# Kernel optimization log

Hardware: AMD Instinct MI355X
Metric: run time of the kernel (lower is better)

## Reference

```python
import jax, jax.numpy as jnp
import numpy as np

NB = 2        # trm_num_blocks
H = 4         # trm_num_heads
D = 128       # trm_hidden_dim
L = 512
B = 1
PAD = 0
NEG = jnp.float32(-2**32 + 1)


def _ln(x, g, b, eps=1e-8):
    m = x.mean(-1, keepdims=True)
    v = x.var(-1, keepdims=True)
    return (x - m) / jnp.sqrt(v + eps) * g + b


def setup_inputs() -> dict:
    key = jax.random.key(0)
    ks = jax.random.split(key, 16)
    s = 0.02
    inp = {
        "log_seqs": jax.random.randint(ks[0], (B, L), 0, 1000),
        "seqs": jax.random.normal(ks[1], (B, L, D), jnp.float32),
        "time_matrix_K": jax.random.normal(ks[2], (B, L, L, D), jnp.float32),
        # per-block stacked params [NB, ...]
        "Wq": jax.random.normal(ks[3], (NB, D, D), jnp.float32) * s,
        "bq": jnp.zeros((NB, D), jnp.float32),
        "Wk": jax.random.normal(ks[4], (NB, D, D), jnp.float32) * s,
        "bk": jnp.zeros((NB, D), jnp.float32),
        "Wv": jax.random.normal(ks[5], (NB, D, D), jnp.float32) * s,
        "bv": jnp.zeros((NB, D), jnp.float32),
        "Wt": jax.random.normal(ks[6], (NB, D, D), jnp.float32) * s,
        "bt": jnp.zeros((NB, D), jnp.float32),
        "Wtp": jax.random.normal(ks[7], (NB, D, 1), jnp.float32) * s,
        "btp": jnp.zeros((NB, 1), jnp.float32),
        "ln1_g": jnp.ones((NB, D), jnp.float32),
        "ln1_b": jnp.zeros((NB, D), jnp.float32),
        "ln2_g": jnp.ones((NB, D), jnp.float32),
        "ln2_b": jnp.zeros((NB, D), jnp.float32),
        "W1": jax.random.normal(ks[8], (NB, D, D), jnp.float32) * s,
        "b1": jnp.zeros((NB, D), jnp.float32),
        "W2": jax.random.normal(ks[9], (NB, D, D), jnp.float32) * s,
        "b2": jnp.zeros((NB, D), jnp.float32),
        "lnf_g": jnp.ones((D,), jnp.float32),
        "lnf_b": jnp.zeros((D,), jnp.float32),
    }
    return inp


def reference(log_seqs, seqs, time_matrix_K, Wq, bq, Wk, bk, Wv, bv, Wt, bt,
              Wtp, btp, ln1_g, ln1_b, ln2_g, ln2_b, W1, b1, W2, b2, lnf_g, lnf_b):
    hd = D // H
    pad = (log_seqs == PAD)                     # [B, L] True at padding
    keep = (~pad)[..., None].astype(seqs.dtype)  # [B, L, 1]
    seqs = seqs * keep
    causal = ~jnp.tril(jnp.ones((L, L), bool))  # True above diagonal (masked)
    # combined mask [1, B, L, L]: pad query rows OR non-causal entries
    mask = pad[None, :, :, None] | causal[None, None, :, :]

    attn_ws = []
    for i in range(NB):
        Q = _ln(seqs, ln1_g[i], ln1_b[i])
        q = Q @ Wq[i] + bq[i]
        k = seqs @ Wk[i] + bk[i]
        v = seqs @ Wv[i] + bv[i]
        # head-major layout [H, B, L, hd] (matches torch split+cat along dim 0)
        qh = q.reshape(B, L, H, hd).transpose(2, 0, 1, 3)
        kh = k.reshape(B, L, H, hd).transpose(2, 0, 1, 3)
        vh = v.reshape(B, L, H, hd).transpose(2, 0, 1, 3)
        scores = jnp.einsum('hbqd,hbkd->hbqk', qh, kh)  # [H, B, L, L]
        # time bias: sigmoid(proj(relu(W_t t))) in (0,1); log is negative
        tw = jax.nn.sigmoid(
            (jax.nn.relu(time_matrix_K @ Wt[i] + bt[i]) @ Wtp[i] + btp[i]).squeeze(-1)
        )                                             # [B, L, L]
        scores = (scores + jnp.log(tw)) / jnp.float32(hd) ** 0.5
        scores = jnp.where(mask, NEG, scores)
        w = jax.nn.softmax(scores, axis=-1)           # dropout is identity (eval)
        attn_ws.append(w.reshape(H * B, L, L))
        out = jnp.einsum('hbqk,hbkd->hbqd', w, vh).transpose(1, 2, 0, 3).reshape(B, L, D)
        seqs = Q + out
        x = _ln(seqs, ln2_g[i], ln2_b[i])
        y = jax.nn.relu(x @ W1[i] + b1[i]) @ W2[i] + b2[i]
        seqs = (x + y) * keep                         # FFN residual adds post-LN x
    log_feats = _ln(seqs, lnf_g, lnf_b)
    return (log_feats, tuple(attn_ws))
```

## Files before the change

kernel.cpp:

```cpp
#include <hip/hip_runtime.h>

#define L 512
#define D 128
#define H 4
#define HD 32
#define XLD 132

typedef __bf16 bf16x8 __attribute__((ext_vector_type(8)));
typedef float  f32x4  __attribute__((ext_vector_type(4)));

__device__ __forceinline__ unsigned short bfbits(float v){
  __bf16 h = (__bf16)v; unsigned short u; __builtin_memcpy(&u, &h, 2); return u;
}
__device__ __forceinline__ bf16x8 cvt8(float4 a0, float4 a1){
  bf16x8 r;
  r[0] = (__bf16)a0.x; r[1] = (__bf16)a0.y; r[2] = (__bf16)a0.z; r[3] = (__bf16)a0.w;
  r[4] = (__bf16)a1.x; r[5] = (__bf16)a1.y; r[6] = (__bf16)a1.z; r[7] = (__bf16)a1.w;
  return r;
}

__device__ __forceinline__ void write_qA(unsigned short* qA, int row, int c, float v){
  int qt = row >> 4, m = row & 15;
  int h = c >> 5, cc = c & 31;
  qA[(((qt * 4 + h) * 64) + (cc >> 3) * 16 + m) * 8 + (cc & 7)] = bfbits(v);
}
__device__ __forceinline__ void write_kB(unsigned short* kB, int row, int c, float v){
  int h = c >> 5, cc = c & 31;
  int nt = row >> 4;
  kB[((h * 32 + nt) * 64 + (cc >> 3) * 16 + (row & 15)) * 8 + (cc & 7)] = bfbits(v);
}
__device__ __forceinline__ void write_vB(unsigned short* vB, int row, int c, float v){
  int h = c >> 5, cc = c & 31;
  int kk = row >> 5, qv = (row >> 3) & 3, jv = row & 7;
  int nt = cc >> 4;
  vB[(((h * 16 + kk) * 2 + nt) * 64 + qv * 16 + (cc & 15)) * 8 + jv] = bfbits(v);
}

__device__ __forceinline__ void row_stats16(const float (*buf)[XLD], int tid,
                                            float* mean_s, float* rstd_s){
  int row_l = tid >> 4, seg = tid & 15;
  const float* p = &buf[row_l][seg * 8];
  float4 f0 = *(const float4*)p, f1 = *(const float4*)(p + 4);
  float sum = f0.x + f0.y + f0.z + f0.w + f1.x + f1.y + f1.z + f1.w;
  float sq  = f0.x*f0.x + f0.y*f0.y + f0.z*f0.z + f0.w*f0.w
            + f1.x*f1.x + f1.y*f1.y + f1.z*f1.z + f1.w*f1.w;
#pragma unroll
  for (int o = 1; o < 16; o <<= 1){ sum += __shfl_xor(sum, o); sq += __shfl_xor(sq, o); }
  if (seg == 0){
    float mn = sum * (1.f / 128.f);
    mean_s[row_l] = mn;
    rstd_s[row_l] = rsqrtf(fmaxf(sq * (1.f / 128.f) - mn * mn, 0.f) + 1e-8f);
  }
}

__device__ __forceinline__ void build_afr(const float (*buf)[XLD], int lane, bf16x8* afr){
  int m = lane & 15, quad = lane >> 4;
#pragma unroll
  for (int k0 = 0; k0 < 4; ++k0){
    const float* p = &buf[m][k0 * 32 + quad * 8];
    afr[k0] = cvt8(*(const float4*)p, *(const float4*)(p + 4));
  }
}
__device__ __forceinline__ void build_afr_ln(const float (*buf)[XLD], int lane,
    const float* mean_s, const float* rstd_s,
    const float* __restrict__ g, const float* __restrict__ b, bf16x8* afr){
  int m = lane & 15, quad = lane >> 4;
  float mn = mean_s[m], rs = rstd_s[m];
#pragma unroll
  for (int k0 = 0; k0 < 4; ++k0){
    int c0 = k0 * 32 + quad * 8;
    const float* p = &buf[m][c0];
    float4 a0 = *(const float4*)p, a1 = *(const float4*)(p + 4);
    float q[8];
    q[0]=(a0.x-mn)*rs*g[c0+0]+b[c0+0]; q[1]=(a0.y-mn)*rs*g[c0+1]+b[c0+1];
    q[2]=(a0.z-mn)*rs*g[c0+2]+b[c0+2]; q[3]=(a0.w-mn)*rs*g[c0+3]+b[c0+3];
    q[4]=(a1.x-mn)*rs*g[c0+4]+b[c0+4]; q[5]=(a1.y-mn)*rs*g[c0+5]+b[c0+5];
    q[6]=(a1.z-mn)*rs*g[c0+6]+b[c0+6]; q[7]=(a1.w-mn)*rs*g[c0+7]+b[c0+7];
    bf16x8 r;
    r[0]=(__bf16)q[0]; r[1]=(__bf16)q[1]; r[2]=(__bf16)q[2]; r[3]=(__bf16)q[3];
    r[4]=(__bf16)q[4]; r[5]=(__bf16)q[5]; r[6]=(__bf16)q[6]; r[7]=(__bf16)q[7];
    afr[k0] = r;
  }
}

__global__ void k_prep(const float* __restrict__ Wt,
                       const float* __restrict__ Wq, const float* __restrict__ Wk,
                       const float* __restrict__ Wv, const float* __restrict__ W1,
                       const float* __restrict__ W2,
                       unsigned short* __restrict__ bfg, unsigned short* __restrict__ wf){
  int idx = blockIdx.x * 256 + threadIdx.x;
  if (idx < 32768){
    int jj   = idx & 7;
    int lane = (idx >> 3) & 63;
    int k0   = (idx >> 9) & 3;
    int nt   = idx >> 11;
    int d    = k0 * 32 + (lane >> 4) * 8 + jj;
    int col  = (nt & 7) * 16 + (lane & 15);
    int blk  = nt >> 3;
    bfg[idx] = bfbits(Wt[blk * D * D + d * D + col]);
  } else {
    int i2 = idx - 32768;
    int jj = i2 & 7, lane = (i2 >> 3) & 63, k0 = (i2 >> 9) & 3, nt = (i2 >> 11) & 7;
    int mat = i2 >> 14;
    int blk = mat / 5, m5 = mat % 5;
    const float* W = (m5 == 0 ? Wq : m5 == 1 ? Wk : m5 == 2 ? Wv : m5 == 3 ? W1 : W2)
                     + blk * D * D;
    int d = k0 * 32 + (lane >> 4) * 8 + jj;
    int col = nt * 16 + (lane & 15);
    wf[i2] = bfbits(W[d * D + col]);
  }
}

__global__ __launch_bounds__(256, 2) void k_timebias(
    const float* __restrict__ T, const unsigned short* __restrict__ bfg,
    const float* __restrict__ bt, const float* __restrict__ wtp,
    const float* __restrict__ btp, float* __restrict__ logtw){
  __shared__ __align__(16) unsigned short bsh[16384];
  __shared__ float bts[128], wtps[128];
  int tid = threadIdx.x;
  int lane = tid & 63, w = tid >> 6;
  int quad = lane >> 4, m = lane & 15;
  const bf16x8* bls = (const bf16x8*)bsh;
  int wbase = blockIdx.x * 256 + w * 64;

  bf16x8 afr[4][4];
#pragma unroll
  for (int mt = 0; mt < 4; ++mt){
    const float* tp = T + (size_t)(wbase + mt * 16 + m) * D + quad * 8;
#pragma unroll
    for (int k0 = 0; k0 < 4; ++k0){
      float4 f0 = *(const float4*)(tp + k0 * 32);
      float4 f1 = *(const float4*)(tp + k0 * 32 + 4);
      afr[mt][k0] = cvt8(f0, f1);
    }
  }

#pragma unroll
  for (int blk = 0; blk < 2; ++blk){
    if (blk) __syncthreads();
    {
      const uint4* g = (const uint4*)(bfg + blk * 16384);
      uint4* s = (uint4*)bsh;
#pragma unroll
      for (int i = 0; i < 8; ++i) s[tid + i * 256] = g[tid + i * 256];
      if (tid < 128){ bts[tid] = bt[blk * 128 + tid]; wtps[tid] = wtp[blk * 128 + tid]; }
    }
    __syncthreads();

    f32x4 rs[4] = {{0,0,0,0},{0,0,0,0},{0,0,0,0},{0,0,0,0}};
#pragma unroll
    for (int ntl = 0; ntl < 8; ++ntl){
      f32x4 acc[4] = {{0,0,0,0},{0,0,0,0},{0,0,0,0},{0,0,0,0}};
#pragma unroll
      for (int k0 = 0; k0 < 4; ++k0){
        bf16x8 b = bls[(ntl * 4 + k0) * 64 + lane];
#pragma unroll
        for (int mt = 0; mt < 4; ++mt)
          acc[mt] = __builtin_amdgcn_mfma_f32_16x16x32_bf16(afr[mt][k0], b, acc[mt], 0, 0, 0);
      }
      float btv = bts[ntl * 16 + m];
      float wtv = wtps[ntl * 16 + m];
#pragma unroll
      for (int mt = 0; mt < 4; ++mt)
#pragma unroll
        for (int r = 0; r < 4; ++r)
          rs[mt][r] += fmaxf(acc[mt][r] + btv, 0.f) * wtv;
    }
#pragma unroll
    for (int mt = 0; mt < 4; ++mt)
#pragma unroll
      for (int r = 0; r < 4; ++r){
        float v = rs[mt][r];
        v += __shfl_xor(v, 1); v += __shfl_xor(v, 2);
        v += __shfl_xor(v, 4); v += __shfl_xor(v, 8);
        rs[mt][r] = v;
      }
    if (m == 0){
      float bp = btp[blk];
      float* out = logtw + blk * (L * L);
#pragma unroll
      for (int mt = 0; mt < 4; ++mt){
        float4 o;
        float s0 = rs[mt][0] + bp; o.x = -__logf(1.f + __expf(-s0));
        float s1 = rs[mt][1] + bp; o.y = -__logf(1.f + __expf(-s1));
        float s2 = rs[mt][2] + bp; o.z = -__logf(1.f + __expf(-s2));
        float s3 = rs[mt][3] + bp; o.w = -__logf(1.f + __expf(-s3));
        *(float4*)(out + wbase + mt * 16 + quad * 4) = o;
      }
    }
  }
}

__global__ __launch_bounds__(256) void k_qkv_m(
    const float* __restrict__ src, const int* __restrict__ ls, int domask,
    const float* __restrict__ g1, const float* __restrict__ b1,
    const unsigned short* __restrict__ wf, int matq,
    const float* __restrict__ bq, const float* __restrict__ bk,
    const float* __restrict__ bv,
    float* __restrict__ Q, unsigned short* __restrict__ qA,
    unsigned short* __restrict__ kB, unsigned short* __restrict__ vB){
  __shared__ float xs[16][XLD];
  __shared__ float mean_s[16], rstd_s[16];
  __shared__ float g1s[128], b1s[128];
  int tid = threadIdx.x, rowbase = blockIdx.x * 16;
  int mat = blockIdx.y;
  int row_l = tid >> 4, seg = tid & 15;

  const float* sp = src + (rowbase + row_l) * D + seg * 8;
  float4 f0 = *(const float4*)sp, f1 = *(const float4*)(sp + 4);
  if (domask && ls[rowbase + row_l] == 0){
    f0 = make_float4(0,0,0,0); f1 = make_float4(0,0,0,0);
  }
  *(float4*)&xs[row_l][seg * 8] = f0;
  *(float4*)&xs[row_l][seg * 8 + 4] = f1;
  if (mat == 0 && tid < 128){ g1s[tid] = g1[tid]; b1s[tid] = b1[tid]; }
  __syncthreads();
  if (mat == 0){
    row_stats16(xs, tid, mean_s, rstd_s);
    __syncthreads();
    float mn = mean_s[row_l], rs = rstd_s[row_l];
    float* qp = Q + (rowbase + row_l) * D + seg * 8;
    float4 o0, o1;
    int c0 = seg * 8;
    o0.x=(f0.x-mn)*rs*g1s[c0+0]+b1s[c0+0]; o0.y=(f0.y-mn)*rs*g1s[c0+1]+b1s[c0+1];
    o0.z=(f0.z-mn)*rs*g1s[c0+2]+b1s[c0+2]; o0.w=(f0.w-mn)*rs*g1s[c0+3]+b1s[c0+3];
    o1.x=(f1.x-mn)*rs*g1s[c0+4]+b1s[c0+4]; o1.y=(f1.y-mn)*rs*g1s[c0+5]+b1s[c0+5];
    o1.z=(f1.z-mn)*rs*g1s[c0+6]+b1s[c0+6]; o1.w=(f1.w-mn)*rs*g1s[c0+7]+b1s[c0+7];
    *(float4*)qp = o0; *(float4*)(qp + 4) = o1;
  }

  int lane = tid & 63, w = tid >> 6;
  int quad = lane >> 4, mcol = lane & 15;
  bf16x8 afr[4];
  if (mat == 0) build_afr_ln(xs, lane, mean_s, rstd_s, g1s, b1s, afr);
  else          build_afr(xs, lane, afr);

  const float* bias_v = (mat == 0 ? bq : mat == 1 ? bk : bv);
#pragma unroll
  for (int jl = 0; jl < 2; ++jl){
    int nt = w * 2 + jl;
    const bf16x8* wfb = (const bf16x8*)wf + ((size_t)(matq + mat) * 8 + nt) * 4 * 64;
    f32x4 acc = {0, 0, 0, 0};
#pragma unroll
    for (int k0 = 0; k0 < 4; ++k0)
      acc = __builtin_amdgcn_mfma_f32_16x16x32_bf16(afr[k0], wfb[k0 * 64 + lane], acc, 0, 0, 0);
    int c = nt * 16 + mcol;
    float bias = bias_v[c];
#pragma unroll
    for (int r = 0; r < 4; ++r){
      int row = rowbase + quad * 4 + r;
      float v = acc[r] + bias;
      if (mat == 0) write_qA(qA, row, c, v);
      else if (mat == 1) write_kB(kB, row, c, v);
      else write_vB(vB, row, c, v);
    }
  }
}

__global__ __launch_bounds__(256) void k_attn(
    const unsigned short* __restrict__ qA, const unsigned short* __restrict__ kB,
    const unsigned short* __restrict__ vB, const float* __restrict__ logtw,
    const int* __restrict__ ls, const float* __restrict__ Q,
    float* __restrict__ wout, float* __restrict__ xr){
  __shared__ __align__(16) unsigned short pa[16 * 64 * 8];
  __shared__ float pvp[4][2][64][4];
  __shared__ float smax[4][16], ssum[4][16];
  int qt = blockIdx.x >> 2, h = blockIdx.x & 3;
  int tid = threadIdx.x, lane = tid & 63, w = tid >> 6;
  int quad = lane >> 4, mcol = lane & 15;
  const float RS = 0.17677669529663687f;

  bf16x8 qf = ((const bf16x8*)qA)[(qt * 4 + h) * 64 + lane];

  f32x4 acc[8];
#pragma unroll
  for (int nt8 = 0; nt8 < 8; ++nt8){
    bf16x8 bf = ((const bf16x8*)kB)[(h * 32 + w * 8 + nt8) * 64 + lane];
    f32x4 z = {0, 0, 0, 0};
    acc[nt8] = __builtin_amdgcn_mfma_f32_16x16x32_bf16(qf, bf, z, 0, 0, 0);
  }

  float e[8][4];
  float mx4[4] = {-3e38f, -3e38f, -3e38f, -3e38f};
#pragma unroll
  for (int nt8 = 0; nt8 < 8; ++nt8){
    int col = w * 128 + nt8 * 16 + mcol;
#pragma unroll
    for (int r = 0; r < 4; ++r){
      int row = qt * 16 + quad * 4 + r;
      float sv = (acc[nt8][r] + logtw[row * L + col]) * RS;
      sv = (col <= row) ? sv : -3e38f;
      e[nt8][r] = sv;
      mx4[r] = fmaxf(mx4[r], sv);
    }
  }
#pragma unroll
  for (int r = 0; r < 4; ++r){
    float v = mx4[r];
    v = fmaxf(v, __shfl_xor(v, 1)); v = fmaxf(v, __shfl_xor(v, 2));
    v = fmaxf(v, __shfl_xor(v, 4)); v = fmaxf(v, __shfl_xor(v, 8));
    mx4[r] = v;
  }
  if (mcol == 0){
#pragma unroll
    for (int r = 0; r < 4; ++r) smax[w][quad * 4 + r] = mx4[r];
  }
  __syncthreads();
  float mxr[4], sum4[4] = {0, 0, 0, 0};
#pragma unroll
  for (int r = 0; r < 4; ++r){
    int rr = quad * 4 + r;
    mxr[r] = fmaxf(fmaxf(smax[0][rr], smax[1][rr]), fmaxf(smax[2][rr], smax[3][rr]));
  }
#pragma unroll
  for (int nt8 = 0; nt8 < 8; ++nt8)
#pragma unroll
    for (int r = 0; r < 4; ++r){
      float sv = e[nt8][r];
      float ev = (sv > -1e38f) ? __expf(sv - mxr[r]) : 0.f;
      e[nt8][r] = ev;
      sum4[r] += ev;
    }
#pragma unroll
  for (int r = 0; r < 4; ++r){
    float v = sum4[r];
    v += __shfl_xor(v, 1); v += __shfl_xor(v, 2);
    v += __shfl_xor(v, 4); v += __shfl_xor(v, 8);
    sum4[r] = v;
  }
  if (mcol == 0){
#pragma unroll
    for (int r = 0; r < 4; ++r) ssum[w][quad * 4 + r] = sum4[r];
  }
  __syncthreads();
  float inv[4]; int padr[4];
#pragma unroll
  for (int r = 0; r < 4; ++r){
    int rr = quad * 4 + r;
    inv[r] = 1.f / (ssum[0][rr] + ssum[1][rr] + ssum[2][rr] + ssum[3][rr]);
    padr[r] = (ls[qt * 16 + rr] == 0);
  }
#pragma unroll
  for (int nt8 = 0; nt8 < 8; ++nt8){
    int col = w * 128 + nt8 * 16 + mcol;
    int kk = col >> 5, qk = (col >> 3) & 3, jj = col & 7;
#pragma unroll
    for (int r = 0; r < 4; ++r){
      int rl = quad * 4 + r;
      float wv = padr[r] ? (1.f / 512.f) : e[nt8][r] * inv[r];
      wout[h * (L * L) + (qt * 16 + rl) * L + col] = wv;
      pa[(kk * 64 + qk * 16 + rl) * 8 + jj] = bfbits(wv);
    }
  }

  f32x4 pacc[2] = {{0,0,0,0},{0,0,0,0}};
#pragma unroll
  for (int kk4 = 0; kk4 < 4; ++kk4){
    int kk = w * 4 + kk4;
    bf16x8 af = ((const bf16x8*)pa)[kk * 64 + lane];
#pragma unroll
    for (int nt = 0; nt < 2; ++nt){
      bf16x8 bf = ((const bf16x8*)vB)[((h * 16 + kk) * 2 + nt) * 64 + lane];
      pacc[nt] = __builtin_amdgcn_mfma_f32_16x16x32_bf16(af, bf, pacc[nt], 0, 0, 0);
    }
  }
#pragma unroll
  for (int nt = 0; nt < 2; ++nt)
#pragma unroll
    for (int r = 0; r < 4; ++r) pvp[w][nt][lane][r] = pacc[nt][r];
  __syncthreads();
  if (w < 2){
    int nt = w;
#pragma unroll
    for (int r = 0; r < 4; ++r){
      float o = pvp[0][nt][lane][r] + pvp[1][nt][lane][r]
              + pvp[2][nt][lane][r] + pvp[3][nt][lane][r];
      int row = qt * 16 + quad * 4 + r;
      int cg = h * HD + nt * 16 + mcol;
      xr[row * D + cg] = Q[row * D + cg] + o;
    }
  }
}

__global__ __launch_bounds__(256) void k_ffn_m(
    const float* __restrict__ xr, const int* __restrict__ ls,
    const float* __restrict__ g2, const float* __restrict__ b2,
    const unsigned short* __restrict__ wf, int mat1,
    const float* __restrict__ b1f, const float* __restrict__ b2f,
    int fuse_qkv, const float* __restrict__ g1, const float* __restrict__ b1,
    int matq, const float* __restrict__ bq, const float* __restrict__ bk,
    const float* __restrict__ bv,
    float* __restrict__ Q, unsigned short* __restrict__ qA,
    unsigned short* __restrict__ kB, unsigned short* __restrict__ vB,
    int fuse_lnf, const float* __restrict__ lg, const float* __restrict__ lb,
    float* __restrict__ lf){
  __shared__ float xs[16][XLD];
  __shared__ float x2s[16][XLD];
  __shared__ float y1s[16][XLD];
  __shared__ float xos[16][XLD];
  __shared__ float mean_s[16], rstd_s[16];
  __shared__ float gs[128], bs[128];
  int tid = threadIdx.x, rowbase = blockIdx.x * 16;
  int row_l = tid >> 4, seg = tid & 15;
  int lane = tid & 63, w = tid >> 6;
  int quad = lane >> 4, mcol = lane & 15;

  {
    const float* sp = xr + (rowbase + row_l) * D + seg * 8;
    *(float4*)&xs[row_l][seg * 8] = *(const float4*)sp;
    *(float4*)&xs[row_l][seg * 8 + 4] = *(const float4*)(sp + 4);
    if (tid < 128){ gs[tid] = g2[tid]; bs[tid] = b2[tid]; }
  }
  __syncthreads();
  row_stats16(xs, tid, mean_s, rstd_s);
  __syncthreads();
  {
    float mn = mean_s[row_l], rs = rstd_s[row_l];
#pragma unroll
    for (int i = 0; i < 8; ++i){
      int c = seg * 8 + i;
      x2s[row_l][c] = (xs[row_l][c] - mn) * rs * gs[c] + bs[c];
    }
  }
  __syncthreads();

  bf16x8 afr[4];
  build_afr(x2s, lane, afr);
#pragma unroll
  for (int jl = 0; jl < 2; ++jl){
    int nt = w * 2 + jl;
    const bf16x8* wfb = (const bf16x8*)wf + ((size_t)mat1 * 8 + nt) * 4 * 64;
    f32x4 acc = {0, 0, 0, 0};
#pragma unroll
    for (int k0 = 0; k0 < 4; ++k0)
      acc = __builtin_amdgcn_mfma_f32_16x16x32_bf16(afr[k0], wfb[k0 * 64 + lane], acc, 0, 0, 0);
    int c = nt * 16 + mcol;
    float bias = b1f[c];
#pragma unroll
    for (int r = 0; r < 4; ++r)
      y1s[quad * 4 + r][c] = fmaxf(acc[r] + bias, 0.f);
  }
  __syncthreads();

  build_afr(y1s, lane, afr);
#pragma unroll
  for (int jl = 0; jl < 2; ++jl){
    int nt = w * 2 + jl;
    const bf16x8* wfb = (const bf16x8*)wf + ((size_t)(mat1 + 1) * 8 + nt) * 4 * 64;
    f32x4 acc = {0, 0, 0, 0};
#pragma unroll
    for (int k0 = 0; k0 < 4; ++k0)
      acc = __builtin_amdgcn_mfma_f32_16x16x32_bf16(afr[k0], wfb[k0 * 64 + lane], acc, 0, 0, 0);
    int c = nt * 16 + mcol;
    float bias = b2f[c];
#pragma unroll
    for (int r = 0; r < 4; ++r){
      int rl = quad * 4 + r;
      float kp = (ls[rowbase + rl] != 0) ? 1.f : 0.f;
      xos[rl][c] = (x2s[rl][c] + acc[r] + bias) * kp;
    }
  }
  __syncthreads();

  if (fuse_qkv){
    if (tid < 128){ gs[tid] = g1[tid]; bs[tid] = b1[tid]; }
    row_stats16(xos, tid, mean_s, rstd_s);
    __syncthreads();
    {
      float mn = mean_s[row_l], rs = rstd_s[row_l];
      float* qp = Q + (rowbase + row_l) * D + seg * 8;
      float4 o0, o1;
      int c0 = seg * 8;
      o0.x=(xos[row_l][c0+0]-mn)*rs*gs[c0+0]+bs[c0+0];
      o0.y=(xos[row_l][c0+1]-mn)*rs*gs[c0+1]+bs[c0+1];
      o0.z=(xos[row_l][c0+2]-mn)*rs*gs[c0+2]+bs[c0+2];
      o0.w=(xos[row_l][c0+3]-mn)*rs*gs[c0+3]+bs[c0+3];
      o1.x=(xos[row_l][c0+4]-mn)*rs*gs[c0+4]+bs[c0+4];
      o1.y=(xos[row_l][c0+5]-mn)*rs*gs[c0+5]+bs[c0+5];
      o1.z=(xos[row_l][c0+6]-mn)*rs*gs[c0+6]+bs[c0+6];
      o1.w=(xos[row_l][c0+7]-mn)*rs*gs[c0+7]+bs[c0+7];
      *(float4*)qp = o0; *(float4*)(qp + 4) = o1;
    }
    bf16x8 afrQ[4], afrX[4];
    build_afr_ln(xos, lane, mean_s, rstd_s, gs, bs, afrQ);
    build_afr(xos, lane, afrX);
#pragma unroll
    for (int jl = 0; jl < 6; ++jl){
      int j = w * 6 + jl;
      int mat = j >> 3, nt = j & 7;
      const bf16x8* wfb = (const bf16x8*)wf + ((size_t)(matq + mat) * 8 + nt) * 4 * 64;
      f32x4 acc = {0, 0, 0, 0};
#pragma unroll
      for (int k0 = 0; k0 < 4; ++k0)
        acc = __builtin_amdgcn_mfma_f32_16x16x32_bf16(mat == 0 ? afrQ[k0] : afrX[k0],
                                                      wfb[k0 * 64 + lane], acc, 0, 0, 0);
      int c = nt * 16 + mcol;
      float bias = (mat == 0 ? bq : mat == 1 ? bk : bv)[c];
#pragma unroll
      for (int r = 0; r < 4; ++r){
        int row = rowbase + quad * 4 + r;
        float v = acc[r] + bias;
        if (mat == 0) write_qA(qA, row, c, v);
        else if (mat == 1) write_kB(kB, row, c, v);
        else write_vB(vB, row, c, v);
      }
    }
  }

  if (fuse_lnf){
    if (tid < 128){ gs[tid] = lg[tid]; bs[tid] = lb[tid]; }
    row_stats16(xos, tid, mean_s, rstd_s);
    __syncthreads();
    float mn = mean_s[row_l], rs = rstd_s[row_l];
    float* op = lf + (rowbase + row_l) * D + seg * 8;
    float4 o0, o1;
    int c0 = seg * 8;
    o0.x=(xos[row_l][c0+0]-mn)*rs*gs[c0+0]+bs[c0+0];
    o0.y=(xos[row_l][c0+1]-mn)*rs*gs[c0+1]+bs[c0+1];
    o0.z=(xos[row_l][c0+2]-mn)*rs*gs[c0+2]+bs[c0+2];
    o0.w=(xos[row_l][c0+3]-mn)*rs*gs[c0+3]+bs[c0+3];
    o1.x=(xos[row_l][c0+4]-mn)*rs*gs[c0+4]+bs[c0+4];
    o1.y=(xos[row_l][c0+5]-mn)*rs*gs[c0+5]+bs[c0+5];
    o1.z=(xos[row_l][c0+6]-mn)*rs*gs[c0+6]+bs[c0+6];
    o1.w=(xos[row_l][c0+7]-mn)*rs*gs[c0+7]+bs[c0+7];
    *(float4*)op = o0; *(float4*)(op + 4) = o1;
  }
}

extern "C" void kernel_launch(void* const* d_in, const int* in_sizes, int n_in,
                              void* d_out, int out_size, void* d_ws, size_t ws_size,
                              hipStream_t stream){
  const int*   ls   = (const int*)d_in[0];
  const float* seqs = (const float*)d_in[1];
  const float* T    = (const float*)d_in[2];
  const float* Wq   = (const float*)d_in[3];
  const float* bq   = (const float*)d_in[4];
  const float* Wk   = (const float*)d_in[5];
  const float* bk   = (const float*)d_in[6];
  const float* Wv   = (const float*)d_in[7];
  const float* bv   = (const float*)d_in[8];
  const float* Wt   = (const float*)d_in[9];
  const float* bt   = (const float*)d_in[10];
  const float* Wtp  = (const float*)d_in[11];
  const float* btp  = (const float*)d_in[12];
  const float* g1   = (const float*)d_in[13];
  const float* b1   = (const float*)d_in[14];
  const float* g2   = (const float*)d_in[15];
  const float* b2   = (const float*)d_in[16];
  const float* W1   = (const float*)d_in[17];
  const float* b1f  = (const float*)d_in[18];
  const float* W2   = (const float*)d_in[19];
  const float* b2f  = (const float*)d_in[20];
  const float* lg   = (const float*)d_in[21];
  const float* lb   = (const float*)d_in[22];

  float* ws    = (float*)d_ws;
  float* Q     = ws;
  float* xr    = Q + 65536;
  float* logtw = xr + 65536;
  unsigned short* bfg = (unsigned short*)(logtw + 2 * 262144);
  unsigned short* wf  = bfg + 32768;
  unsigned short* qA  = wf + 163840;
  unsigned short* kB  = qA + 65536;
  unsigned short* vB  = kB + 65536;

  float* outF = (float*)d_out;
  float* lf = outF;
  float* w0 = outF + 65536;
  float* w1 = w0 + 1048576;

  k_prep    <<<768, 256, 0, stream>>>(Wt, Wq, Wk, Wv, W1, W2, bfg, wf);
  k_timebias<<<1024, 256, 0, stream>>>(T, bfg, bt, Wtp, btp, logtw);

  k_qkv_m<<<dim3(32, 3), 256, 0, stream>>>(seqs, ls, 1, g1, b1, wf, 0, bq, bk, bv,
                                           Q, qA, kB, vB);
  k_attn<<<128, 256, 0, stream>>>(qA, kB, vB, logtw, ls, Q, w0, xr);
  k_ffn_m<<<32, 256, 0, stream>>>(xr, ls, g2, b2, wf, 3, b1f, b2f,
                                  1, g1 + D, b1 + D, 5, bq + D, bk + D, bv + D,
                                  Q, qA, kB, vB,
                                  0, lg, lb, lf);
  k_attn<<<128, 256, 0, stream>>>(qA, kB, vB, logtw + L * L, ls, Q, w1, xr);
  k_ffn_m<<<32, 256, 0, stream>>>(xr, ls, g2 + D, b2 + D, wf, 8, b1f + D, b2f + D,
                                  0, g1, b1, 0, bq, bk, bv,
                                  Q, qA, kB, vB,
                                  1, lg, lb, lf);
}
```

Before: 276.6 us.

## Skip masked causal tiles in time-bias and attention; merge time-bias with QKV kernel

The time-bias kernel now computes only the lower-triangular 64-wide key strips. 576 blocks cover the causal region instead of 1024 covering the full L×L grid, so most of the large time_matrix read and the MFMA work above the diagonal are skipped. The first QKV projection is folded into the same launch as extra blocks, removing one kernel launch. In attention, waves whose key range lies entirely above the diagonal skip the QK MFMAs, the logtw loads and the PV MFMAs. The risk is that logtw above the diagonal is left unwritten, which is safe only because those entries are always masked.

```diff
diff --git a/kernel.cpp b/kernel.cpp
--- a/kernel.cpp
+++ b/kernel.cpp
@@ -5,6 +5,7 @@
 #define H 4
 #define HD 32
 #define XLD 132
+#define NTB 576
 
 typedef __bf16 bf16x8 __attribute__((ext_vector_type(8)));
 typedef float  f32x4  __attribute__((ext_vector_type(4)));
@@ -111,104 +112,115 @@
   }
 }
 
-__global__ __launch_bounds__(256, 2) void k_timebias(
+__global__ __launch_bounds__(256, 2) void k_tb_qkv(
     const float* __restrict__ T, const unsigned short* __restrict__ bfg,
     const float* __restrict__ bt, const float* __restrict__ wtp,
-    const float* __restrict__ btp, float* __restrict__ logtw){
-  __shared__ __align__(16) unsigned short bsh[16384];
-  __shared__ float bts[128], wtps[128];
-  int tid = threadIdx.x;
-  int lane = tid & 63, w = tid >> 6;
-  int quad = lane >> 4, m = lane & 15;
-  const bf16x8* bls = (const bf16x8*)bsh;
-  int wbase = blockIdx.x * 256 + w * 64;
-
-  bf16x8 afr[4][4];
-#pragma unroll
-  for (int mt = 0; mt < 4; ++mt){
-    const float* tp = T + (size_t)(wbase + mt * 16 + m) * D + quad * 8;
-#pragma unroll
-    for (int k0 = 0; k0 < 4; ++k0){
-      float4 f0 = *(const float4*)(tp + k0 * 32);
-      float4 f1 = *(const float4*)(tp + k0 * 32 + 4);
-      afr[mt][k0] = cvt8(f0, f1);
-    }
-  }
-
-#pragma unroll
-  for (int blk = 0; blk < 2; ++blk){
-    if (blk) __syncthreads();
-    {
-      const uint4* g = (const uint4*)(bfg + blk * 16384);
-      uint4* s = (uint4*)bsh;
-#pragma unroll
-      for (int i = 0; i < 8; ++i) s[tid + i * 256] = g[tid + i * 256];
-      if (tid < 128){ bts[tid] = bt[blk * 128 + tid]; wtps[tid] = wtp[blk * 128 + tid]; }
-    }
-    __syncthreads();
-
-    f32x4 rs[4] = {{0,0,0,0},{0,0,0,0},{0,0,0,0},{0,0,0,0}};
-#pragma unroll
-    for (int ntl = 0; ntl < 8; ++ntl){
-      f32x4 acc[4] = {{0,0,0,0},{0,0,0,0},{0,0,0,0},{0,0,0,0}};
-#pragma unroll
-      for (int k0 = 0; k0 < 4; ++k0){
-        bf16x8 b = bls[(ntl * 4 + k0) * 64 + lane];
-#pragma unroll
-        for (int mt = 0; mt < 4; ++mt)
-          acc[mt] = __builtin_amdgcn_mfma_f32_16x16x32_bf16(afr[mt][k0], b, acc[mt], 0, 0, 0);
-      }
-      float btv = bts[ntl * 16 + m];
-      float wtv = wtps[ntl * 16 + m];
-#pragma unroll
-      for (int mt = 0; mt < 4; ++mt)
-#pragma unroll
-        for (int r = 0; r < 4; ++r)
-          rs[mt][r] += fmaxf(acc[mt][r] + btv, 0.f) * wtv;
-    }
-#pragma unroll
-    for (int mt = 0; mt < 4; ++mt)
-#pragma unroll
-      for (int r = 0; r < 4; ++r){
-        float v = rs[mt][r];
-        v += __shfl_xor(v, 1); v += __shfl_xor(v, 2);
-        v += __shfl_xor(v, 4); v += __shfl_xor(v, 8);
-        rs[mt][r] = v;
-      }
-    if (m == 0){
-      float bp = btp[blk];
-      float* out = logtw + blk * (L * L);
-#pragma unroll
-      for (int mt = 0; mt < 4; ++mt){
-        float4 o;
-        float s0 = rs[mt][0] + bp; o.x = -__logf(1.f + __expf(-s0));
-        float s1 = rs[mt][1] + bp; o.y = -__logf(1.f + __expf(-s1));
-        float s2 = rs[mt][2] + bp; o.z = -__logf(1.f + __expf(-s2));
-        float s3 = rs[mt][3] + bp; o.w = -__logf(1.f + __expf(-s3));
-        *(float4*)(out + wbase + mt * 16 + quad * 4) = o;
-      }
-    }
-  }
-}
-
-__global__ __launch_bounds__(256) void k_qkv_m(
-    const float* __restrict__ src, const int* __restrict__ ls, int domask,
+    const float* __restrict__ btp, float* __restrict__ logtw,
+    const float* __restrict__ src, const int* __restrict__ ls,
     const float* __restrict__ g1, const float* __restrict__ b1,
-    const unsigned short* __restrict__ wf, int matq,
+    const unsigned short* __restrict__ wf,
     const float* __restrict__ bq, const float* __restrict__ bk,
     const float* __restrict__ bv,
     float* __restrict__ Q, unsigned short* __restrict__ qA,
     unsigned short* __restrict__ kB, unsigned short* __restrict__ vB){
+  __shared__ __align__(16) unsigned short bsh[16384];
+  __shared__ float bts[128], wtps[128];
   __shared__ float xs[16][XLD];
   __shared__ float mean_s[16], rstd_s[16];
   __shared__ float g1s[128], b1s[128];
-  int tid = threadIdx.x, rowbase = blockIdx.x * 16;
-  int mat = blockIdx.y;
+  int tid = threadIdx.x;
+  int lane = tid & 63, w = tid >> 6;
+  int quad = lane >> 4;
+
+  if (blockIdx.x < NTB){
+    int m = lane & 15;
+    const bf16x8* bls = (const bf16x8*)bsh;
+    int strip = blockIdx.x * 4 + w;
+    int b = 0;
+#pragma unroll
+    for (int i = 1; i < 8; ++i) if (strip >= 32 * i * (i + 1)) b = i;
+    int r0 = strip - 32 * b * (b + 1);
+    int q  = b * 64 + r0 / (b + 1);
+    int kb = (r0 % (b + 1)) * 64;
+    int wbase = q * L + kb;
+
+    bf16x8 afr[4][4];
+#pragma unroll
+    for (int mt = 0; mt < 4; ++mt){
+      const float* tp = T + (size_t)(wbase + mt * 16 + m) * D + quad * 8;
+#pragma unroll
+      for (int k0 = 0; k0 < 4; ++k0){
+        float4 f0 = *(const float4*)(tp + k0 * 32);
+        float4 f1 = *(const float4*)(tp + k0 * 32 + 4);
+        afr[mt][k0] = cvt8(f0, f1);
+      }
+    }
+
+#pragma unroll
+    for (int blk = 0; blk < 2; ++blk){
+      if (blk) __syncthreads();
+      {
+        const uint4* g = (const uint4*)(bfg + blk * 16384);
+        uint4* s = (uint4*)bsh;
+#pragma unroll
+        for (int i = 0; i < 8; ++i) s[tid + i * 256] = g[tid + i * 256];
+        if (tid < 128){ bts[tid] = bt[blk * 128 + tid]; wtps[tid] = wtp[blk * 128 + tid]; }
+      }
+      __syncthreads();
+
+      f32x4 rs[4] = {{0,0,0,0},{0,0,0,0},{0,0,0,0},{0,0,0,0}};
+#pragma unroll
+      for (int ntl = 0; ntl < 8; ++ntl){
+        f32x4 acc[4] = {{0,0,0,0},{0,0,0,0},{0,0,0,0},{0,0,0,0}};
+#pragma unroll
+        for (int k0 = 0; k0 < 4; ++k0){
+          bf16x8 bfr = bls[(ntl * 4 + k0) * 64 + lane];
+#pragma unroll
+          for (int mt = 0; mt < 4; ++mt)
+            acc[mt] = __builtin_amdgcn_mfma_f32_16x16x32_bf16(afr[mt][k0], bfr, acc[mt], 0, 0, 0);
+        }
+        float btv = bts[ntl * 16 + m];
+        float wtv = wtps[ntl * 16 + m];
+#pragma unroll
+        for (int mt = 0; mt < 4; ++mt)
+#pragma unroll
+          for (int r = 0; r < 4; ++r)
+            rs[mt][r] += fmaxf(acc[mt][r] + btv, 0.f) * wtv;
+      }
+#pragma unroll
+      for (int mt = 0; mt < 4; ++mt)
+#pragma unroll
+        for (int r = 0; r < 4; ++r){
+          float v = rs[mt][r];
+          v += __shfl_xor(v, 1); v += __shfl_xor(v, 2);
+          v += __shfl_xor(v, 4); v += __shfl_xor(v, 8);
+          rs[mt][r] = v;
+        }
+      if (m == 0){
+        float bp = btp[blk];
+        float* out = logtw + blk * (L * L);
+#pragma unroll
+        for (int mt = 0; mt < 4; ++mt){
+          float4 o;
+          float s0 = rs[mt][0] + bp; o.x = -__logf(1.f + __expf(-s0));
+          float s1 = rs[mt][1] + bp; o.y = -__logf(1.f + __expf(-s1));
+          float s2 = rs[mt][2] + bp; o.z = -__logf(1.f + __expf(-s2));
+          float s3 = rs[mt][3] + bp; o.w = -__logf(1.f + __expf(-s3));
+          *(float4*)(out + wbase + mt * 16 + quad * 4) = o;
+        }
+      }
+    }
+    return;
+  }
+
+  int bi = blockIdx.x - NTB;
+  int rowbase = (bi & 31) * 16;
+  int mat = bi >> 5;
   int row_l = tid >> 4, seg = tid & 15;
 
   const float* sp = src + (rowbase + row_l) * D + seg * 8;
   float4 f0 = *(const float4*)sp, f1 = *(const float4*)(sp + 4);
-  if (domask && ls[rowbase + row_l] == 0){
+  if (ls[rowbase + row_l] == 0){
     f0 = make_float4(0,0,0,0); f1 = make_float4(0,0,0,0);
   }
   *(float4*)&xs[row_l][seg * 8] = f0;
@@ -229,8 +241,7 @@
     *(float4*)qp = o0; *(float4*)(qp + 4) = o1;
   }
 
-  int lane = tid & 63, w = tid >> 6;
-  int quad = lane >> 4, mcol = lane & 15;
+  int mcol = lane & 15;
   bf16x8 afr[4];
   if (mat == 0) build_afr_ln(xs, lane, mean_s, rstd_s, g1s, b1s, afr);
   else          build_afr(xs, lane, afr);
@@ -239,7 +250,7 @@
 #pragma unroll
   for (int jl = 0; jl < 2; ++jl){
     int nt = w * 2 + jl;
-    const bf16x8* wfb = (const bf16x8*)wf + ((size_t)(matq + mat) * 8 + nt) * 4 * 64;
+    const bf16x8* wfb = (const bf16x8*)wf + ((size_t)mat * 8 + nt) * 4 * 64;
     f32x4 acc = {0, 0, 0, 0};
 #pragma unroll
     for (int k0 = 0; k0 < 4; ++k0)
@@ -269,31 +280,41 @@
   int tid = threadIdx.x, lane = tid & 63, w = tid >> 6;
   int quad = lane >> 4, mcol = lane & 15;
   const float RS = 0.17677669529663687f;
-
-  bf16x8 qf = ((const bf16x8*)qA)[(qt * 4 + h) * 64 + lane];
-
-  f32x4 acc[8];
-#pragma unroll
-  for (int nt8 = 0; nt8 < 8; ++nt8){
-    bf16x8 bf = ((const bf16x8*)kB)[(h * 32 + w * 8 + nt8) * 64 + lane];
-    f32x4 z = {0, 0, 0, 0};
-    acc[nt8] = __builtin_amdgcn_mfma_f32_16x16x32_bf16(qf, bf, z, 0, 0, 0);
-  }
+  int row_max = qt * 16 + 15;
+  bool skipw = (w * 128) > row_max;
 
   float e[8][4];
+  if (!skipw){
+    bf16x8 qf = ((const bf16x8*)qA)[(qt * 4 + h) * 64 + lane];
+    f32x4 acc[8];
+#pragma unroll
+    for (int nt8 = 0; nt8 < 8; ++nt8){
+      bf16x8 bf = ((const bf16x8*)kB)[(h * 32 + w * 8 + nt8) * 64 + lane];
+      f32x4 z = {0, 0, 0, 0};
+      acc[nt8] = __builtin_amdgcn_mfma_f32_16x16x32_bf16(qf, bf, z, 0, 0, 0);
+    }
+#pragma unroll
+    for (int nt8 = 0; nt8 < 8; ++nt8){
+      int col = w * 128 + nt8 * 16 + mcol;
+#pragma unroll
+      for (int r = 0; r < 4; ++r){
+        int row = qt * 16 + quad * 4 + r;
+        float sv = (acc[nt8][r] + logtw[row * L + col]) * RS;
+        e[nt8][r] = (col <= row) ? sv : -3e38f;
+      }
+    }
+  } else {
+#pragma unroll
+    for (int nt8 = 0; nt8 < 8; ++nt8)
+#pragma unroll
+      for (int r = 0; r < 4; ++r) e[nt8][r] = -3e38f;
+  }
+
   float mx4[4] = {-3e38f, -3e38f, -3e38f, -3e38f};
 #pragma unroll
-  for (int nt8 = 0; nt8 < 8; ++nt8){
-    int col = w * 128 + nt8 * 16 + mcol;
-#pragma unroll
-    for (int r = 0; r < 4; ++r){
-      int row = qt * 16 + quad * 4 + r;
-      float sv = (acc[nt8][r] + logtw[row * L + col]) * RS;
-      sv = (col <= row) ? sv : -3e38f;
-      e[nt8][r] = sv;
-      mx4[r] = fmaxf(mx4[r], sv);
-    }
-  }
+  for (int nt8 = 0; nt8 < 8; ++nt8)
+#pragma unroll
+    for (int r = 0; r < 4; ++r) mx4[r] = fmaxf(mx4[r], e[nt8][r]);
 #pragma unroll
   for (int r = 0; r < 4; ++r){
     float v = mx4[r];
@@ -349,19 +370,21 @@
       int rl = quad * 4 + r;
       float wv = padr[r] ? (1.f / 512.f) : e[nt8][r] * inv[r];
       wout[h * (L * L) + (qt * 16 + rl) * L + col] = wv;
-      pa[(kk * 64 + qk * 16 + rl) * 8 + jj] = bfbits(wv);
+      if (!skipw) pa[(kk * 64 + qk * 16 + rl) * 8 + jj] = bfbits(wv);
     }
   }
 
   f32x4 pacc[2] = {{0,0,0,0},{0,0,0,0}};
-#pragma unroll
-  for (int kk4 = 0; kk4 < 4; ++kk4){
-    int kk = w * 4 + kk4;
-    bf16x8 af = ((const bf16x8*)pa)[kk * 64 + lane];
-#pragma unroll
-    for (int nt = 0; nt < 2; ++nt){
-      bf16x8 bf = ((const bf16x8*)vB)[((h * 16 + kk) * 2 + nt) * 64 + lane];
-      pacc[nt] = __builtin_amdgcn_mfma_f32_16x16x32_bf16(af, bf, pacc[nt], 0, 0, 0);
+  if (!skipw){
+#pragma unroll
+    for (int kk4 = 0; kk4 < 4; ++kk4){
+      int kk = w * 4 + kk4;
+      bf16x8 af = ((const bf16x8*)pa)[kk * 64 + lane];
+#pragma unroll
+      for (int nt = 0; nt < 2; ++nt){
+        bf16x8 bf = ((const bf16x8*)vB)[((h * 16 + kk) * 2 + nt) * 64 + lane];
+        pacc[nt] = __builtin_amdgcn_mfma_f32_16x16x32_bf16(af, bf, pacc[nt], 0, 0, 0);
+      }
     }
   }
 #pragma unroll
@@ -569,11 +592,10 @@
   float* w0 = outF + 65536;
   float* w1 = w0 + 1048576;
 
-  k_prep    <<<768, 256, 0, stream>>>(Wt, Wq, Wk, Wv, W1, W2, bfg, wf);
-  k_timebias<<<1024, 256, 0, stream>>>(T, bfg, bt, Wtp, btp, logtw);
-
-  k_qkv_m<<<dim3(32, 3), 256, 0, stream>>>(seqs, ls, 1, g1, b1, wf, 0, bq, bk, bv,
-                                           Q, qA, kB, vB);
+  k_prep  <<<768, 256, 0, stream>>>(Wt, Wq, Wk, Wv, W1, W2, bfg, wf);
+  k_tb_qkv<<<NTB + 96, 256, 0, stream>>>(T, bfg, bt, Wtp, btp, logtw,
+                                         seqs, ls, g1, b1, wf, bq, bk, bv,
+                                         Q, qA, kB, vB);
   k_attn<<<128, 256, 0, stream>>>(qA, kB, vB, logtw, ls, Q, w0, xr);
   k_ffn_m<<<32, 256, 0, stream>>>(xr, ls, g2, b2, wf, 3, b1f, b2f,
                                   1, g1 + D, b1 + D, 5, bq + D, bk + D, bv + D,
```

Measured after the change: 267.3 us (median of 2 runs). 1.03x faster.
